# Kernel tuning notes

Hardware: AMD Instinct MI355X
Metric: run time of the kernel (lower is better)

The kernel has to match this reference:

```python
import jax, jax.numpy as jnp
import numpy as np

MAXLEN = 100  # target_node_incoming_edge_maxlim in to_dense_batch_JY


def setup_inputs() -> dict:
    key = jax.random.key(0)
    ks = jax.random.split(key, 6)
    N, F, H, B = 500000, 64, 64, 8192
    x = jax.random.normal(ks[0], (N, F), dtype=jnp.float32)
    index = jnp.sort(jax.random.randint(ks[1], (N,), 0, B)).astype(jnp.int64)
    s = 1.0 / np.sqrt(H)  # torch LSTM reset_parameters: U(-1/sqrt(H), 1/sqrt(H))
    W_ih = jax.random.uniform(ks[2], (4 * H, F), jnp.float32, -s, s)
    W_hh = jax.random.uniform(ks[3], (4 * H, H), jnp.float32, -s, s)
    b_ih = jax.random.uniform(ks[4], (4 * H,), jnp.float32, -s, s)
    b_hh = jax.random.uniform(ks[5], (4 * H,), jnp.float32, -s, s)
    return {"x": x, "W_ih": W_ih, "W_hh": W_hh, "b_ih": b_ih, "b_hh": b_hh,
            "index": index, "dim_size": B}


def _lstm_last_hidden(dense, mask, W_ih, W_hh, b_ih, b_hh):
    """Run a single-layer LSTM over dense [B,L,F]; freeze state where mask is
    False, which reproduces pack_sequence semantics (ht = hidden at last valid
    step of each sequence; zero-length sequences stay at h0=0)."""
    B, L, F = dense.shape
    H = W_hh.shape[1]
    # input projection for all timesteps at once: [B, L, 4H]
    xg = jnp.einsum('blf,gf->blg', dense, W_ih) + (b_ih + b_hh)

    def step(carry, inp):
        h, c = carry
        g_x, m = inp                      # g_x: [B,4H], m: [B] bool
        g = g_x + h @ W_hh.T
        i, f, gc, o = jnp.split(g, 4, axis=-1)  # torch gate order: i, f, g, o
        i = jax.nn.sigmoid(i)
        f = jax.nn.sigmoid(f)
        gc = jnp.tanh(gc)
        o = jax.nn.sigmoid(o)
        c_new = f * c + i * gc
        h_new = o * jnp.tanh(c_new)
        m2 = m[:, None]
        return (jnp.where(m2, h_new, h), jnp.where(m2, c_new, c)), None

    h0 = jnp.zeros((B, H), dense.dtype)
    (h, _c), _ = jax.lax.scan(step, (h0, h0),
                              (jnp.swapaxes(xg, 0, 1), mask.T))
    return h  # [B, H] == ht[-1]


def reference(x, W_ih, W_hh, b_ih, b_hh, index, dim_size):
    N, F = x.shape
    index = index.astype(jnp.int32)
    # per-graph node counts and exclusive-cumsum offsets (index is sorted)
    counts = jax.ops.segment_sum(jnp.ones(N, jnp.int32), index,
                                 num_segments=dim_size)
    offsets = jnp.concatenate([jnp.zeros(1, jnp.int32),
                               jnp.cumsum(counts)[:-1].astype(jnp.int32)])
    pos = jnp.arange(N, dtype=jnp.int32) - offsets[index]  # position in graph
    valid = pos < MAXLEN                                   # truncate to 100
    # scatter into dense [B, MAXLEN, F]; invalid rows are zeroed and added at
    # slot 0 so they are no-ops
    dense = jnp.zeros((dim_size, MAXLEN, F), x.dtype)
    dense = dense.at[index, jnp.where(valid, pos, 0)].add(
        jnp.where(valid[:, None], x, 0.0))
    seq_len = jnp.minimum(counts, MAXLEN)
    mask = jnp.arange(MAXLEN)[None, :] < seq_len[:, None]  # [B, MAXLEN]
    return _lstm_last_hidden(dense, mask, W_ih, W_hh, b_ih, b_hh)
```

## Files before the change

kernel.cpp:

```cpp
#include <hip/hip_runtime.h>

#define MAXLEN 100
#define HDIM 64
#define CH 8
#define NSEG 12
#define SROW 72
#define SPLANE (CH * SROW + 8)
#define HSTR 72
#define L2E 1.44269504f

typedef __attribute__((ext_vector_type(8))) short bf16x8;
typedef __attribute__((ext_vector_type(4))) float f32x4;

#define LGKM_BARRIER() asm volatile("s_waitcnt lgkmcnt(0)\n\ts_barrier" ::: "memory")

__device__ __forceinline__ unsigned short f2bf_u(float f) {
    unsigned u = __float_as_uint(f);
    u += 0x7fffu + ((u >> 16) & 1u);
    return (unsigned short)(u >> 16);
}
__device__ __forceinline__ unsigned pk2(float a, float b) {
    return (unsigned)f2bf_u(a) | ((unsigned)f2bf_u(b) << 16);
}
__device__ __forceinline__ bf16x8 pack8(f32x4 a, f32x4 b) {
    union { unsigned u[4]; bf16x8 v; } c;
    c.u[0] = pk2(a[0], a[1]); c.u[1] = pk2(a[2], a[3]);
    c.u[2] = pk2(b[0], b[1]); c.u[3] = pk2(b[2], b[3]);
    return c.v;
}
__device__ __forceinline__ float sig_b(float v, float bs) {
    return __builtin_amdgcn_rcpf(1.0f + __builtin_amdgcn_exp2f(fmaf(v, -L2E, bs)));
}
__device__ __forceinline__ float tanh_b(float v, float bs2) {
    return fmaf(2.0f, __builtin_amdgcn_rcpf(1.0f + __builtin_amdgcn_exp2f(fmaf(v, -2.0f * L2E, bs2))), -1.0f);
}
__device__ __forceinline__ float tanh_p(float v) {
    return fmaf(2.0f, __builtin_amdgcn_rcpf(1.0f + __builtin_amdgcn_exp2f(v * (-2.0f * L2E))), -1.0f);
}

__global__ __launch_bounds__(256, 3)
void lstm12_kernel(const float* __restrict__ x,
                   const float* __restrict__ Wih,
                   const float* __restrict__ Whh,
                   const float* __restrict__ bih,
                   const float* __restrict__ bhh,
                   const int* __restrict__ index,
                   float* __restrict__ out, int N, int B) {
    const int tid  = threadIdx.x;
    const int w    = tid >> 6;
    const int lane = tid & 63;
    const int l15  = lane & 15;
    const int quad = lane >> 4;
    const int segbase = blockIdx.x * NSEG;
    const int ncol = w * 16 + l15;

    __shared__ __align__(16) unsigned short xst[NSEG * SPLANE];
    __shared__ __align__(16) unsigned short hst[2][16][HSTR];
    __shared__ int sstart[NSEG], slen[NSEG];

    if (tid < NSEG) {
        const int b = segbase + tid;
        int s = 0, len = 0;
        if (b < B) {
            int lo = 0, hi = N;
            while (lo < hi) { int m = (lo + hi) >> 1; if (index[m] < b) lo = m + 1; else hi = m; }
            s = lo;
            hi = N;
            while (lo < hi) { int m = (lo + hi) >> 1; if (index[m] < b + 1) lo = m + 1; else hi = m; }
            len = lo - s;
            len = len < MAXLEN ? len : MAXLEN;
        }
        sstart[tid] = s;
        slen[tid] = len;
    }
    for (int i = tid; i < 2 * 16 * HSTR / 2; i += 256) ((int*)hst)[i] = 0;
    __syncthreads();

    bf16x8 wi[4][2], wh[4][2];
    float bs[4];
#pragma unroll
    for (int g = 0; g < 4; ++g) {
        const int row = g * HDIM + ncol;
        const float bb = bih[row] + bhh[row];
        bs[g] = (g == 2) ? (-2.0f * L2E) * bb : (-L2E) * bb;
#pragma unroll
        for (int kt = 0; kt < 2; ++kt) {
            const f32x4* pi = (const f32x4*)(Wih + (size_t)row * HDIM + kt * 32 + quad * 8);
            const f32x4* ph = (const f32x4*)(Whh + (size_t)row * HDIM + kt * 32 + quad * 8);
            wi[g][kt] = pack8(pi[0], pi[1]);
            wh[g][kt] = pack8(ph[0], ph[1]);
        }
    }

    int len3[3];
#pragma unroll
    for (int r = 0; r < 3; ++r) len3[r] = slen[quad * 3 + r];
    int lmax = 0;
#pragma unroll
    for (int i = 0; i < NSEG; ++i) { int v = slen[i]; lmax = v > lmax ? v : lmax; }
    lmax = __builtin_amdgcn_readfirstlane(lmax);

    const int ustep = (tid >> 3) & 7, ugrp = tid & 7;
    const int us0 = tid >> 6;
    int sst3[3], sln3[3];
#pragma unroll
    for (int k = 0; k < 3; ++k) { sst3[k] = sstart[us0 + 4 * k]; sln3[k] = slen[us0 + 4 * k]; }

    f32x4 pre[3][2];

#define ISSUE(t0_)                                                              \
    {                                                                           \
        _Pragma("unroll")                                                       \
        for (int k_ = 0; k_ < 3; ++k_) {                                        \
            int ct = (t0_) + ustep;                                             \
            ct = (sln3[k_] > 0) ? (ct < sln3[k_] ? ct : sln3[k_] - 1) : 0;      \
            int row = sst3[k_] + ct;                                            \
            row = row < N - 1 ? row : N - 1;                                    \
            const f32x4* p_ = (const f32x4*)(x + (size_t)row * HDIM + ugrp * 8);\
            pre[k_][0] = p_[0]; pre[k_][1] = p_[1];                             \
        }                                                                       \
    }
#define COMMIT()                                                                \
    {                                                                           \
        _Pragma("unroll")                                                       \
        for (int k_ = 0; k_ < 3; ++k_) {                                        \
            uint4 o_;                                                           \
            o_.x = pk2(pre[k_][0][0], pre[k_][0][1]);                           \
            o_.y = pk2(pre[k_][0][2], pre[k_][0][3]);                           \
            o_.z = pk2(pre[k_][1][0], pre[k_][1][1]);                           \
            o_.w = pk2(pre[k_][1][2], pre[k_][1][3]);                           \
            *(uint4*)&xst[(us0 + 4 * k_) * SPLANE + ustep * SROW + ugrp * 8] = o_; \
        }                                                                       \
    }

    const int m3 = l15 & 3;
    const int xp = (l15 >> 2) * 3 + (m3 < 2 ? m3 : 2);
    const unsigned short* xb = &xst[xp * SPLANE + quad * 8];

    float c3[3] = {0, 0, 0}, h3[3] = {0, 0, 0};
    const f32x4 cz = {0.0f, 0.0f, 0.0f, 0.0f};
    const int nch = (lmax + CH - 1) / CH;

    if (nch > 0) {
        ISSUE(0);
        COMMIT();
        LGKM_BARRIER();
        if (nch > 1) ISSUE(CH);

        for (int ch = 0; ch < nch; ++ch) {
            const int t0 = ch * CH;
#pragma unroll
            for (int tt = 0; tt < CH; ++tt) {
                const int t = t0 + tt;
                const int pb = tt & 1, nb = pb ^ 1;

                const unsigned short* xr = xb + tt * SROW;
                bf16x8 xa0 = *(const bf16x8*)(xr);
                bf16x8 xa1 = *(const bf16x8*)(xr + 32);
                const unsigned short* hr = &hst[pb][l15][quad * 8];
                bf16x8 ha0 = *(const bf16x8*)(hr);
                bf16x8 ha1 = *(const bf16x8*)(hr + 32);

                f32x4 acc[4];
#pragma unroll
                for (int g = 0; g < 4; ++g) {
                    f32x4 a = __builtin_amdgcn_mfma_f32_16x16x32_bf16(xa0, wi[g][0], cz, 0, 0, 0);
                    a = __builtin_amdgcn_mfma_f32_16x16x32_bf16(xa1, wi[g][1], a, 0, 0, 0);
                    a = __builtin_amdgcn_mfma_f32_16x16x32_bf16(ha0, wh[g][0], a, 0, 0, 0);
                    a = __builtin_amdgcn_mfma_f32_16x16x32_bf16(ha1, wh[g][1], a, 0, 0, 0);
                    acc[g] = a;
                }

#pragma unroll
                for (int r = 0; r < 3; ++r) {
                    float gi = sig_b (acc[0][r], bs[0]);
                    float gf = sig_b (acc[1][r], bs[1]);
                    float gg = tanh_b(acc[2][r], bs[2]);
                    float go = sig_b (acc[3][r], bs[3]);
                    float cn = fmaf(gf, c3[r], gi * gg);
                    float hn = go * tanh_p(cn);
                    const bool up = t < len3[r];
                    c3[r] = up ? cn : c3[r];
                    h3[r] = up ? hn : h3[r];
                    hst[nb][quad * 4 + r][ncol] = f2bf_u(h3[r]);
                }
                LGKM_BARRIER();
            }
            if (ch + 1 < nch) {
                COMMIT();
                LGKM_BARRIER();
                if (ch + 2 < nch) ISSUE((ch + 2) * CH);
            }
        }
    }

#pragma unroll
    for (int r = 0; r < 3; ++r) {
        const int seg = segbase + quad * 3 + r;
        if (seg < B) out[(size_t)seg * HDIM + ncol] = h3[r];
    }
#undef ISSUE
#undef COMMIT
}

extern "C" void kernel_launch(void* const* d_in, const int* in_sizes, int n_in,
                              void* d_out, int out_size, void* d_ws, size_t ws_size,
                              hipStream_t stream) {
    const float* x     = (const float*)d_in[0];
    const float* Wih   = (const float*)d_in[1];
    const float* Whh   = (const float*)d_in[2];
    const float* bih   = (const float*)d_in[3];
    const float* bhh   = (const float*)d_in[4];
    const int*   index = (const int*)d_in[5];

    const int N = in_sizes[5];
    const int B = out_size / HDIM;

    const int nblocks = (B + NSEG - 1) / NSEG;
    lstm12_kernel<<<nblocks, 256, 0, stream>>>(x, Wih, Whh, bih, bhh, index,
                                               (float*)d_out, N, B);
}
```

Before: 258.5 us.

## Precompute next-step input projection off the recurrent critical path, halve chunk size

The input-projection MFMAs (x·W_ih) for step t+1 are now issued right after step t's recurrent MFMAs, so each step's dependency chain only carries the two W_hh MFMAs on h. The chunk of x rows staged in LDS shrinks from 8 to 4 timesteps. The global-to-LDS staging is remapped so three waves each load 64 contiguous bytes per thread, and the fourth wave does no loads. In exchange there are more commit barriers per sequence, and the accx registers are held across the activation phase.

```diff
diff --git a/kernel.cpp b/kernel.cpp
--- a/kernel.cpp
+++ b/kernel.cpp
@@ -2,7 +2,7 @@
 
 #define MAXLEN 100
 #define HDIM 64
-#define CH 8
+#define CH 4
 #define NSEG 12
 #define SROW 72
 #define SPLANE (CH * SROW + 8)
@@ -100,42 +100,48 @@
     for (int i = 0; i < NSEG; ++i) { int v = slen[i]; lmax = v > lmax ? v : lmax; }
     lmax = __builtin_amdgcn_readfirstlane(lmax);
 
-    const int ustep = (tid >> 3) & 7, ugrp = tid & 7;
-    const int us0 = tid >> 6;
-    int sst3[3], sln3[3];
-#pragma unroll
-    for (int k = 0; k < 3; ++k) { sst3[k] = sstart[us0 + 4 * k]; sln3[k] = slen[us0 + 4 * k]; }
-
-    f32x4 pre[3][2];
+    const int sS = tid >> 4, sT = (tid >> 2) & 3, sC = tid & 3;
+    const int sst = (tid < 192) ? sstart[sS] : 0;
+    const int sln = (tid < 192) ? slen[sS] : 0;
+
+    f32x4 pre[4];
 
 #define ISSUE(t0_)                                                              \
-    {                                                                           \
-        _Pragma("unroll")                                                       \
-        for (int k_ = 0; k_ < 3; ++k_) {                                        \
-            int ct = (t0_) + ustep;                                             \
-            ct = (sln3[k_] > 0) ? (ct < sln3[k_] ? ct : sln3[k_] - 1) : 0;      \
-            int row = sst3[k_] + ct;                                            \
-            row = row < N - 1 ? row : N - 1;                                    \
-            const f32x4* p_ = (const f32x4*)(x + (size_t)row * HDIM + ugrp * 8);\
-            pre[k_][0] = p_[0]; pre[k_][1] = p_[1];                             \
-        }                                                                       \
+    if (w < 3) {                                                                \
+        int ct = (t0_) + sT;                                                    \
+        ct = (sln > 0) ? (ct < sln ? ct : sln - 1) : 0;                         \
+        int row = sst + ct;                                                     \
+        row = row < N - 1 ? row : N - 1;                                        \
+        const f32x4* p_ = (const f32x4*)(x + (size_t)row * HDIM + sC * 16);     \
+        pre[0] = p_[0]; pre[1] = p_[1]; pre[2] = p_[2]; pre[3] = p_[3];         \
     }
 #define COMMIT()                                                                \
-    {                                                                           \
-        _Pragma("unroll")                                                       \
-        for (int k_ = 0; k_ < 3; ++k_) {                                        \
-            uint4 o_;                                                           \
-            o_.x = pk2(pre[k_][0][0], pre[k_][0][1]);                           \
-            o_.y = pk2(pre[k_][0][2], pre[k_][0][3]);                           \
-            o_.z = pk2(pre[k_][1][0], pre[k_][1][1]);                           \
-            o_.w = pk2(pre[k_][1][2], pre[k_][1][3]);                           \
-            *(uint4*)&xst[(us0 + 4 * k_) * SPLANE + ustep * SROW + ugrp * 8] = o_; \
-        }                                                                       \
+    if (w < 3) {                                                                \
+        uint4 o1, o2;                                                           \
+        o1.x = pk2(pre[0][0], pre[0][1]); o1.y = pk2(pre[0][2], pre[0][3]);     \
+        o1.z = pk2(pre[1][0], pre[1][1]); o1.w = pk2(pre[1][2], pre[1][3]);     \
+        o2.x = pk2(pre[2][0], pre[2][1]); o2.y = pk2(pre[2][2], pre[2][3]);     \
+        o2.z = pk2(pre[3][0], pre[3][1]); o2.w = pk2(pre[3][2], pre[3][3]);     \
+        unsigned short* d_ = &xst[sS * SPLANE + sT * SROW + sC * 16];           \
+        *(uint4*)d_ = o1; *(uint4*)(d_ + 8) = o2;                               \
     }
 
     const int m3 = l15 & 3;
     const int xp = (l15 >> 2) * 3 + (m3 < 2 ? m3 : 2);
     const unsigned short* xb = &xst[xp * SPLANE + quad * 8];
+
+    f32x4 accx[4];
+#define ACCX(tt_)                                                               \
+    {                                                                           \
+        const unsigned short* xr_ = xb + (tt_) * SROW;                          \
+        bf16x8 xa0_ = *(const bf16x8*)(xr_);                                    \
+        bf16x8 xa1_ = *(const bf16x8*)(xr_ + 32);                               \
+        _Pragma("unroll")                                                       \
+        for (int g_ = 0; g_ < 4; ++g_) {                                        \
+            f32x4 a_ = __builtin_amdgcn_mfma_f32_16x16x32_bf16(xa0_, wi[g_][0], cz, 0, 0, 0); \
+            accx[g_] = __builtin_amdgcn_mfma_f32_16x16x32_bf16(xa1_, wi[g_][1], a_, 0, 0, 0); \
+        }                                                                       \
+    }
 
     float c3[3] = {0, 0, 0}, h3[3] = {0, 0, 0};
     const f32x4 cz = {0.0f, 0.0f, 0.0f, 0.0f};
@@ -145,6 +151,7 @@
         ISSUE(0);
         COMMIT();
         LGKM_BARRIER();
+        ACCX(0);
         if (nch > 1) ISSUE(CH);
 
         for (int ch = 0; ch < nch; ++ch) {
@@ -154,9 +161,6 @@
                 const int t = t0 + tt;
                 const int pb = tt & 1, nb = pb ^ 1;
 
-                const unsigned short* xr = xb + tt * SROW;
-                bf16x8 xa0 = *(const bf16x8*)(xr);
-                bf16x8 xa1 = *(const bf16x8*)(xr + 32);
                 const unsigned short* hr = &hst[pb][l15][quad * 8];
                 bf16x8 ha0 = *(const bf16x8*)(hr);
                 bf16x8 ha1 = *(const bf16x8*)(hr + 32);
@@ -164,12 +168,11 @@
                 f32x4 acc[4];
 #pragma unroll
                 for (int g = 0; g < 4; ++g) {
-                    f32x4 a = __builtin_amdgcn_mfma_f32_16x16x32_bf16(xa0, wi[g][0], cz, 0, 0, 0);
-                    a = __builtin_amdgcn_mfma_f32_16x16x32_bf16(xa1, wi[g][1], a, 0, 0, 0);
-                    a = __builtin_amdgcn_mfma_f32_16x16x32_bf16(ha0, wh[g][0], a, 0, 0, 0);
-                    a = __builtin_amdgcn_mfma_f32_16x16x32_bf16(ha1, wh[g][1], a, 0, 0, 0);
-                    acc[g] = a;
+                    f32x4 a = __builtin_amdgcn_mfma_f32_16x16x32_bf16(ha0, wh[g][0], accx[g], 0, 0, 0);
+                    acc[g] = __builtin_amdgcn_mfma_f32_16x16x32_bf16(ha1, wh[g][1], a, 0, 0, 0);
                 }
+
+                if (tt + 1 < CH) ACCX(tt + 1);
 
 #pragma unroll
                 for (int r = 0; r < 3; ++r) {
@@ -189,6 +192,7 @@
             if (ch + 1 < nch) {
                 COMMIT();
                 LGKM_BARRIER();
+                ACCX(0);
                 if (ch + 2 < nch) ISSUE((ch + 2) * CH);
             }
         }
@@ -201,6 +205,7 @@
     }
 #undef ISSUE
 #undef COMMIT
+#undef ACCX
 }
 
 extern "C" void kernel_launch(void* const* d_in, const int* in_sizes, int n_in,
```

Measured after the change: 250.1 us. -3.2%, faster.
